# Optimization experiments

Hardware: AMD Instinct MI355X
Metric: run time of the kernel (lower is better)

## Reference

```python
import jax, jax.numpy as jnp
import numpy as np

# config matching init_kwargs
J = 5
Q = 8
T = 15
C = 4
J_PHI = 2
B = 4
N = 65536

# near_sym_b level-1 lowpass (13-tap) from the dtcwt library; highpass via QMF modulation.
H0O = np.array([-0.00455690456024, -0.00543947593727, 0.01702522388155, 0.02382538479492,
                -0.10671180468666, 0.01186609203379, 0.56881042071212, 0.75614564389252,
                0.27529538466888, -0.11720388769911, -0.03887280126882, 0.03466034684485,
                -0.00388321199915], dtype=np.float32)
H1O = (((-1.0) ** np.arange(13)) * H0O[::-1]).astype(np.float32)
# qshift_a 10-tap filters for levels >= 2 (tree b = time-reversed tree a)
H0A = np.array([0.03516384, 0.0, -0.08832942, 0.23389032, 0.76027237,
                0.58751830, 0.0, -0.11430184, 0.0, 0.0], dtype=np.float32)
H0B = H0A[::-1].copy()
H1A = (((-1.0) ** np.arange(10)) * H0B).astype(np.float32)
H1B = H1A[::-1].copy()


def _dwconv(x, h, dilation):
    # depthwise 'same' conv; x: (B,C,N), h: (K,) fixed wavelet filter
    c = x.shape[1]
    k = h.shape[0]
    w = jnp.tile(jnp.asarray(h, x.dtype)[None, None, :], (c, 1, 1))
    tot = dilation * (k - 1)
    return jax.lax.conv_general_dilated(
        x, w, (1,), [(tot // 2, tot - tot // 2)], rhs_dilation=(dilation,),
        dimension_numbers=("NCH", "OIH", "NCH"), feature_group_count=c)


def _gconv(x, w, dilation):
    # grouped learnable conv: x (B,C,N), w (Q*C,1,T), groups=C, 'same' padding
    c = x.shape[1]
    t = w.shape[-1]
    tot = dilation * (t - 1)
    return jax.lax.conv_general_dilated(
        x, w, (1,), [(tot // 2, tot - tot // 2)], rhs_dilation=(dilation,),
        dimension_numbers=("NCH", "OIH", "NCH"), feature_group_count=c)


def _udtcwt(x):
    # undecimated dual-tree CWT (a-trous): returns lowpass and J (real, imag) bandpass pairs
    la, lb = x, x
    bps = []
    for j in range(J):
        d = 1 if j == 0 else 2 ** (j - 1)
        if j == 0:
            h0a, h1a, h0b, h1b = H0O, H1O, H0O, H1O
        else:
            h0a, h1a, h0b, h1b = H0A, H1A, H0B, H1B
        bps.append((_dwconv(la, h1a, d), _dwconv(lb, h1b, d)))
        la = _dwconv(la, h0a, d)
        lb = _dwconv(lb, h0b, d)
    return 0.5 * (la + lb), bps


def _downsample(x):
    # J_phi x (near_sym_b lowpass then ::2 decimation)
    for _ in range(J_PHI):
        x = _dwconv(x, H0O, 1)[:, :, ::2]
    return x


def _forward(x, conv_w, roots, beta):
    lp, bps = _udtcwt(x)
    outs = []
    for j in range(J):
        d = 1 if j == 0 else 2 ** (j - 1)
        scale = 2.0 ** (0.5 * j)  # sqrt(2)**j
        r = _gconv(bps[j][0], conv_w[j], d) / scale
        im = _gconv(bps[j][1], conv_w[j], d) / scale
        u = jnp.sqrt(r * r + im * im)  # ModulusStable
        alpha = jax.nn.sigmoid(roots[j])[None, :, None]  # (1, Q*C, 1)
        u = (jnp.maximum(u, -beta) + beta) ** alpha  # PowerStable
        outs.append(_downsample(u))
    return jnp.concatenate(outs, axis=1)  # (B, C*J*Q, N/2**J_phi)


def setup_inputs() -> dict:
    key = jax.random.key(0)
    kx, kw = jax.random.split(key)
    x = jax.random.normal(kx, (B, C, N), dtype=jnp.float32)
    bound = float(1.0 / np.sqrt(T))  # torch Conv1d default init (in/groups=1)
    conv_w = jax.random.uniform(kw, (J, Q * C, 1, T), dtype=jnp.float32, minval=-bound, maxval=bound)
    roots = jnp.ones((J, Q * C), dtype=jnp.float32)  # module inits root to ones
    beta = jnp.full((1,), 0.01, dtype=jnp.float32)
    return {"x": x, "conv_w": conv_w, "roots": roots, "beta": beta}


def reference(x, conv_w, roots, beta):
    return _forward(x, conv_w, roots, beta)
```

## Files before the change

kernel.cpp:

```cpp
#include <hip/hip_runtime.h>
#include <hip/hip_bf16.h>

typedef float v2f __attribute__((ext_vector_type(2)));

#define B_    4
#define C_    4
#define Q_    8
#define J_    5
#define T_    15
#define NSIG  65536
#define N2SIG 32768
#define NOUT  16384
#define NCH   (B_ * C_)

constexpr float H0Oc[13] = {
    -0.00455690456024f, -0.00543947593727f,  0.01702522388155f,  0.02382538479492f,
    -0.10671180468666f,  0.01186609203379f,  0.56881042071212f,  0.75614564389252f,
     0.27529538466888f, -0.11720388769911f, -0.03887280126882f,  0.03466034684485f,
    -0.00388321199915f };
constexpr float H1Oc[13] = {
    -0.00388321199915f, -0.03466034684485f, -0.03887280126882f,  0.11720388769911f,
     0.27529538466888f, -0.75614564389252f,  0.56881042071212f, -0.01186609203379f,
    -0.10671180468666f, -0.02382538479492f,  0.01702522388155f,  0.00543947593727f,
    -0.00455690456024f };
constexpr float H0Ac[10] = {
     0.03516384f, 0.0f, -0.08832942f, 0.23389032f, 0.76027237f,
     0.58751830f, 0.0f, -0.11430184f, 0.0f, 0.0f };
constexpr float H0Bc[10] = {
     0.0f, 0.0f, -0.11430184f, 0.0f, 0.58751830f,
     0.76027237f, 0.23389032f, -0.08832942f, 0.0f, 0.03516384f };
constexpr float H1Ac[10] = {
     0.0f, 0.0f, -0.11430184f, 0.0f, 0.58751830f,
    -0.76027237f, 0.23389032f, 0.08832942f, 0.0f, -0.03516384f };
constexpr float H1Bc[10] = {
    -0.03516384f, 0.0f, 0.08832942f, 0.23389032f, -0.76027237f,
     0.58751830f, 0.0f, -0.11430184f, 0.0f, 0.0f };

struct Gtab { float v[37]; };
constexpr Gtab make_g() {
    Gtab g{};
    for (int n = 0; n < 37; ++n) {
        float s = 0.f;
        for (int k = 0; k < 13; ++k) {
            int l = n - 2 * k;
            if (l >= 0 && l < 13) s += H0Oc[k] * H0Oc[l];
        }
        g.v[n] = s;
    }
    return g;
}
constexpr Gtab cG = make_g();

#define M2    256
#define NUcnt 1057
#define NUP   1064
#define NBcnt 1169
#define NBP   1176
#define S_    1320

#define SMEM_FLOATS (5280 + 2 * NBP)

__device__ __forceinline__ v2f zmask(v2f a, bool ok) {
    if (!ok) { a.x = 0.f; a.y = 0.f; }
    return a;
}

template<int D>
__device__ __forceinline__ void post_stage(
        const v2f* __restrict__ sRI, v2f* __restrict__ U0, v2f* __restrict__ U1,
        const float* __restrict__ cw, const float* __restrict__ roots,
        float beta, int j, int b, int c, int m0, int mt, int tid,
        float* __restrict__ out) {
    const float lg_is = -0.5f * (float)j;
    const float beta2 = beta * exp2f(0.5f * (float)j);
    const int   u_lo  = 4 * m0 - 18;

    for (int g2 = 0; g2 < 2; ++g2) {
        float w[4][T_], al[4], cq[4];
        #pragma unroll
        for (int qq = 0; qq < 4; ++qq) {
            const int o = c * Q_ + g2 * 4 + qq;
            #pragma unroll
            for (int t = 0; t < T_; t++) w[qq][t] = cw[(size_t)(j * 32 + o) * T_ + t];
            al[qq] = 1.f / (1.f + __expf(-roots[j * 32 + o]));
            cq[qq] = al[qq] * lg_is;
        }

        for (int i = tid; i < NUcnt; i += 256) {
            const int n = u_lo + i;
            const bool ok = ((unsigned)n < (unsigned)NSIG);
            const v2f* tp = sRI + (i + 56 - 7 * D);
            v2f taps[T_];
            #pragma unroll
            for (int t = 0; t < T_; t++) taps[t] = tp[t * D];
            float uq[4];
            #pragma unroll
            for (int qq = 0; qq < 4; ++qq) {
                v2f ri; ri.x = 0.f; ri.y = 0.f;
                #pragma unroll
                for (int t = 0; t < T_; t++) ri += w[qq][t] * taps[t];
                float z2 = fmaf(ri.x, ri.x, ri.y * ri.y);
                float us = sqrtf(z2);
                float lg = __log2f(us + beta2);
                float u  = exp2f(fmaf(al[qq], lg, cq[qq]));
                uq[qq] = ok ? u : 0.f;
            }
            v2f p0; p0.x = uq[0]; p0.y = uq[1];
            v2f p1; p1.x = uq[2]; p1.y = uq[3];
            U0[i] = p0; U1[i] = p1;
        }
        __syncthreads();

        {
            const int m = m0 + tid;
            const bool edge = (mt == 0 && tid < 3) || (mt == 63 && tid >= 253);
            #pragma unroll
            for (int qp = 0; qp < 2; ++qp) {
                const v2f* up = qp ? U1 : U0;
                v2f acc; acc.x = 0.f; acc.y = 0.f;
                #pragma unroll
                for (int n = 0; n < 37; ++n) acc += cG.v[n] * up[4 * tid + n];
                if (edge) {
                    v2f a2; a2.x = 0.f; a2.y = 0.f;
                    for (int k = 0; k < 13; ++k) {
                        int p = 2 * m + k - 6;
                        if (p < 0 || p >= N2SIG) continue;
                        v2f v; v.x = 0.f; v.y = 0.f;
                        for (int l = 0; l < 13; ++l)
                            v += H0Oc[l] * up[4 * tid + 2 * k + l];
                        a2 += H0Oc[k] * v;
                    }
                    acc = a2;
                }
                const int o = c * Q_ + g2 * 4 + 2 * qp;
                out[((size_t)b * 160 + j * 32 + o)     * NOUT + m] = acc.x;
                out[((size_t)b * 160 + j * 32 + o + 1) * NOUT + m] = acc.y;
            }
        }
        __syncthreads();
    }
}

__global__ __launch_bounds__(256, 4) void murenn_all(
        const float* __restrict__ x,
        const float* __restrict__ cw,
        const float* __restrict__ roots,
        const float* __restrict__ beta_p,
        float* __restrict__ out) {
    __shared__ __align__(16) float smem[SMEM_FLOATS];
    float* X   = smem;
    float* L1  = smem + S_;
    v2f*   PP0 = (v2f*)smem;
    v2f*   PP1 = (v2f*)(smem + 2 * S_);
    v2f*   U0  = (v2f*)smem;
    v2f*   U1  = (v2f*)(smem + 2 * NUP);
    v2f*   sRI = (v2f*)(smem + 4 * S_);

    const int tid = threadIdx.x;
    const int mt  = blockIdx.x;
    const int ch  = blockIdx.y;
    const int j   = blockIdx.z;
    const int b   = ch >> 2, c = ch & 3;
    const int m0  = mt * M2;
    const int ofs = 4 * m0 - 147;
    const float beta = beta_p[0];
    const float* xc = x + (size_t)ch * NSIG;

    for (int p = tid; p < S_; p += 256) {
        int g = ofs + p;
        X[p] = ((unsigned)g < (unsigned)NSIG) ? xc[g] : 0.f;
    }
    __syncthreads();

    if (j == 0) {
        for (int i = tid; i < NBcnt; i += 256) {
            int p = 73 + i, g = ofs + p;
            float a = 0.f;
            #pragma unroll
            for (int k = 0; k < 13; k++) a += H1Oc[k] * X[p + k - 6];
            if ((unsigned)g >= (unsigned)NSIG) a = 0.f;
            v2f r; r.x = a; r.y = a;
            sRI[i] = r;
        }
    } else {
        for (int p = 6 + tid; p < 1313; p += 256) {
            int g = ofs + p;
            float a = 0.f;
            #pragma unroll
            for (int k = 0; k < 13; k++) a += H0Oc[k] * X[p + k - 6];
            L1[p] = ((unsigned)g < (unsigned)NSIG) ? a : 0.f;
        }
        __syncthreads();
        if (j == 1) {
            for (int i = tid; i < NBcnt; i += 256) {
                int p = 73 + i, g = ofs + p;
                v2f r; r.x = 0.f; r.y = 0.f;
                #pragma unroll
                for (int k = 0; k < 10; k++) {
                    v2f hk; hk.x = H1Ac[k]; hk.y = H1Bc[k];
                    r += hk * L1[p + k - 4];
                }
                sRI[i] = zmask(r, (unsigned)g < (unsigned)NSIG);
            }
        } else {
            for (int p = 10 + tid; p < 1308; p += 256) {
                int g = ofs + p;
                v2f a; a.x = 0.f; a.y = 0.f;
                #pragma unroll
                for (int k = 0; k < 10; k++) {
                    v2f hk; hk.x = H0Ac[k]; hk.y = H0Bc[k];
                    a += hk * L1[p + k - 4];
                }
                PP1[p] = zmask(a, (unsigned)g < (unsigned)NSIG);
            }
            __syncthreads();
            if (j == 2) {
                for (int i = tid; i < NBcnt; i += 256) {
                    int p = 73 + i, g = ofs + p;
                    v2f r; r.x = 0.f; r.y = 0.f;
                    #pragma unroll
                    for (int k = 0; k < 10; k++) {
                        v2f hk; hk.x = H1Ac[k]; hk.y = H1Bc[k];
                        r += hk * PP1[p + 2 * k - 9];
                    }
                    sRI[i] = zmask(r, (unsigned)g < (unsigned)NSIG);
                }
            } else {
                for (int p = 19 + tid; p < 1299; p += 256) {
                    int g = ofs + p;
                    v2f a; a.x = 0.f; a.y = 0.f;
                    #pragma unroll
                    for (int k = 0; k < 10; k++) {
                        v2f hk; hk.x = H0Ac[k]; hk.y = H0Bc[k];
                        a += hk * PP1[p + 2 * k - 9];
                    }
                    PP0[p] = zmask(a, (unsigned)g < (unsigned)NSIG);
                }
                __syncthreads();
                if (j == 3) {
                    for (int i = tid; i < NBcnt; i += 256) {
                        int p = 73 + i, g = ofs + p;
                        v2f r; r.x = 0.f; r.y = 0.f;
                        #pragma unroll
                        for (int k = 0; k < 10; k++) {
                            v2f hk; hk.x = H1Ac[k]; hk.y = H1Bc[k];
                            r += hk * PP0[p + 4 * k - 18];
                        }
                        sRI[i] = zmask(r, (unsigned)g < (unsigned)NSIG);
                    }
                } else {
                    for (int p = 37 + tid; p < 1281; p += 256) {
                        int g = ofs + p;
                        v2f a; a.x = 0.f; a.y = 0.f;
                        #pragma unroll
                        for (int k = 0; k < 10; k++) {
                            v2f hk; hk.x = H0Ac[k]; hk.y = H0Bc[k];
                            a += hk * PP0[p + 4 * k - 18];
                        }
                        PP1[p] = zmask(a, (unsigned)g < (unsigned)NSIG);
                    }
                    __syncthreads();
                    for (int i = tid; i < NBcnt; i += 256) {
                        int p = 73 + i, g = ofs + p;
                        v2f r; r.x = 0.f; r.y = 0.f;
                        #pragma unroll
                        for (int k = 0; k < 10; k++) {
                            v2f hk; hk.x = H1Ac[k]; hk.y = H1Bc[k];
                            r += hk * PP1[p + 8 * k - 36];
                        }
                        sRI[i] = zmask(r, (unsigned)g < (unsigned)NSIG);
                    }
                }
            }
        }
    }
    __syncthreads();

    if (j == 0)      post_stage<1>(sRI, U0, U1, cw, roots, beta, 0, b, c, m0, mt, tid, out);
    else if (j == 1) post_stage<1>(sRI, U0, U1, cw, roots, beta, 1, b, c, m0, mt, tid, out);
    else if (j == 2) post_stage<2>(sRI, U0, U1, cw, roots, beta, 2, b, c, m0, mt, tid, out);
    else if (j == 3) post_stage<4>(sRI, U0, U1, cw, roots, beta, 3, b, c, m0, mt, tid, out);
    else             post_stage<8>(sRI, U0, U1, cw, roots, beta, 4, b, c, m0, mt, tid, out);
}

extern "C" void kernel_launch(void* const* d_in, const int* in_sizes, int n_in,
                              void* d_out, int out_size, void* d_ws, size_t ws_size,
                              hipStream_t stream) {
    (void)in_sizes; (void)n_in; (void)out_size; (void)d_ws; (void)ws_size;
    const float* x     = (const float*)d_in[0];
    const float* cw    = (const float*)d_in[1];
    const float* roots = (const float*)d_in[2];
    const float* beta  = (const float*)d_in[3];
    float* out = (float*)d_out;

    dim3 grid(NOUT / M2, NCH, J_);
    murenn_all<<<grid, 256, 0, stream>>>(x, cw, roots, beta, out);
}
```

Measured before the change: 184.7 us.

## Process all eight Q filters in one pass with bf16-packed intermediate buffer

The post stage used to run two passes of four filters each, re-reading the taps and syncing twice. It now computes all eight filter outputs per sample in a single pass and stores the modulus-power results as packed bf16 pairs in shared memory, so the buffer still fits. Weights are read straight from global/constant memory instead of being held in registers, and launch bounds drop to 3 blocks per SM. This removes one tap reload and a barrier pass, at the cost of bf16 rounding of the intermediate before the decimation filter and more register pressure.

```diff
diff --git a/kernel.cpp b/kernel.cpp
--- a/kernel.cpp
+++ b/kernel.cpp
@@ -55,7 +55,7 @@
 #define NUcnt 1057
 #define NUP   1064
 #define NBcnt 1169
-#define NBP   1176
+#define NBP   1200
 #define S_    1320
 
 #define SMEM_FLOATS (5280 + 2 * NBP)
@@ -64,84 +64,102 @@
     if (!ok) { a.x = 0.f; a.y = 0.f; }
     return a;
 }
+__device__ __forceinline__ unsigned pack2bf(float a, float b) {
+    unsigned ua = __float_as_uint(a) + 0x8000u;
+    unsigned ub = __float_as_uint(b) + 0x8000u;
+    return (ua >> 16) | (ub & 0xffff0000u);
+}
+__device__ __forceinline__ float unpk_lo(unsigned x) { return __uint_as_float(x << 16); }
+__device__ __forceinline__ float unpk_hi(unsigned x) { return __uint_as_float(x & 0xffff0000u); }
 
 template<int D>
 __device__ __forceinline__ void post_stage(
-        const v2f* __restrict__ sRI, v2f* __restrict__ U0, v2f* __restrict__ U1,
+        const v2f* __restrict__ sRI, uint2* __restrict__ UA, uint2* __restrict__ UB,
         const float* __restrict__ cw, const float* __restrict__ roots,
         float beta, int j, int b, int c, int m0, int mt, int tid,
         float* __restrict__ out) {
     const float lg_is = -0.5f * (float)j;
     const float beta2 = beta * exp2f(0.5f * (float)j);
     const int   u_lo  = 4 * m0 - 18;
-
-    for (int g2 = 0; g2 < 2; ++g2) {
-        float w[4][T_], al[4], cq[4];
+    const float* wbase = cw + (size_t)(j * 32 + c * 8) * T_;
+
+    float al[8], cq[8];
+    #pragma unroll
+    for (int q = 0; q < 8; ++q) {
+        al[q] = 1.f / (1.f + __expf(-roots[j * 32 + c * 8 + q]));
+        cq[q] = al[q] * lg_is;
+    }
+
+    for (int i = tid; i < NUcnt; i += 256) {
+        const int n = u_lo + i;
+        const bool ok = ((unsigned)n < (unsigned)NSIG);
+        const v2f* tp = sRI + (i + 56 - 7 * D);
+        v2f tap[T_];
         #pragma unroll
-        for (int qq = 0; qq < 4; ++qq) {
-            const int o = c * Q_ + g2 * 4 + qq;
+        for (int t = 0; t < T_; t++) tap[t] = tp[t * D];
+        float uq[8];
+        #pragma unroll
+        for (int q = 0; q < 8; ++q) {
+            v2f ri; ri.x = 0.f; ri.y = 0.f;
             #pragma unroll
-            for (int t = 0; t < T_; t++) w[qq][t] = cw[(size_t)(j * 32 + o) * T_ + t];
-            al[qq] = 1.f / (1.f + __expf(-roots[j * 32 + o]));
-            cq[qq] = al[qq] * lg_is;
-        }
-
-        for (int i = tid; i < NUcnt; i += 256) {
-            const int n = u_lo + i;
-            const bool ok = ((unsigned)n < (unsigned)NSIG);
-            const v2f* tp = sRI + (i + 56 - 7 * D);
-            v2f taps[T_];
+            for (int t = 0; t < T_; t++) ri += wbase[q * T_ + t] * tap[t];
+            float z2 = fmaf(ri.x, ri.x, ri.y * ri.y);
+            float us = sqrtf(z2);
+            float lg = __log2f(us + beta2);
+            float u  = exp2f(fmaf(al[q], lg, cq[q]));
+            uq[q] = ok ? u : 0.f;
+        }
+        uint2 pa, pb;
+        pa.x = pack2bf(uq[0], uq[1]); pa.y = pack2bf(uq[2], uq[3]);
+        pb.x = pack2bf(uq[4], uq[5]); pb.y = pack2bf(uq[6], uq[7]);
+        UA[i] = pa; UB[i] = pb;
+    }
+    __syncthreads();
+
+    {
+        const int m = m0 + tid;
+        const bool edge = (mt == 0 && tid < 3) || (mt == 63 && tid >= 253);
+        #pragma unroll
+        for (int pl = 0; pl < 2; ++pl) {
+            const uint2* up = pl ? UB : UA;
+            float a0 = 0.f, a1 = 0.f, a2 = 0.f, a3 = 0.f;
             #pragma unroll
-            for (int t = 0; t < T_; t++) taps[t] = tp[t * D];
-            float uq[4];
-            #pragma unroll
-            for (int qq = 0; qq < 4; ++qq) {
-                v2f ri; ri.x = 0.f; ri.y = 0.f;
-                #pragma unroll
-                for (int t = 0; t < T_; t++) ri += w[qq][t] * taps[t];
-                float z2 = fmaf(ri.x, ri.x, ri.y * ri.y);
-                float us = sqrtf(z2);
-                float lg = __log2f(us + beta2);
-                float u  = exp2f(fmaf(al[qq], lg, cq[qq]));
-                uq[qq] = ok ? u : 0.f;
-            }
-            v2f p0; p0.x = uq[0]; p0.y = uq[1];
-            v2f p1; p1.x = uq[2]; p1.y = uq[3];
-            U0[i] = p0; U1[i] = p1;
-        }
-        __syncthreads();
-
-        {
-            const int m = m0 + tid;
-            const bool edge = (mt == 0 && tid < 3) || (mt == 63 && tid >= 253);
-            #pragma unroll
-            for (int qp = 0; qp < 2; ++qp) {
-                const v2f* up = qp ? U1 : U0;
-                v2f acc; acc.x = 0.f; acc.y = 0.f;
-                #pragma unroll
-                for (int n = 0; n < 37; ++n) acc += cG.v[n] * up[4 * tid + n];
-                if (edge) {
-                    v2f a2; a2.x = 0.f; a2.y = 0.f;
-                    for (int k = 0; k < 13; ++k) {
-                        int p = 2 * m + k - 6;
-                        if (p < 0 || p >= N2SIG) continue;
-                        v2f v; v.x = 0.f; v.y = 0.f;
-                        for (int l = 0; l < 13; ++l)
-                            v += H0Oc[l] * up[4 * tid + 2 * k + l];
-                        a2 += H0Oc[k] * v;
-                    }
-                    acc = a2;
-                }
-                const int o = c * Q_ + g2 * 4 + 2 * qp;
-                out[((size_t)b * 160 + j * 32 + o)     * NOUT + m] = acc.x;
-                out[((size_t)b * 160 + j * 32 + o + 1) * NOUT + m] = acc.y;
-            }
-        }
-        __syncthreads();
-    }
-}
-
-__global__ __launch_bounds__(256, 4) void murenn_all(
+            for (int nn = 0; nn < 37; ++nn) {
+                uint2 t = up[4 * tid + nn];
+                a0 = fmaf(cG.v[nn], unpk_lo(t.x), a0);
+                a1 = fmaf(cG.v[nn], unpk_hi(t.x), a1);
+                a2 = fmaf(cG.v[nn], unpk_lo(t.y), a2);
+                a3 = fmaf(cG.v[nn], unpk_hi(t.y), a3);
+            }
+            if (edge) {
+                float e0 = 0.f, e1 = 0.f, e2 = 0.f, e3 = 0.f;
+                for (int k = 0; k < 13; ++k) {
+                    int p = 2 * m + k - 6;
+                    if (p < 0 || p >= N2SIG) continue;
+                    float v0 = 0.f, v1 = 0.f, v2 = 0.f, v3 = 0.f;
+                    for (int l = 0; l < 13; ++l) {
+                        uint2 t = up[4 * tid + 2 * k + l];
+                        v0 = fmaf(H0Oc[l], unpk_lo(t.x), v0);
+                        v1 = fmaf(H0Oc[l], unpk_hi(t.x), v1);
+                        v2 = fmaf(H0Oc[l], unpk_lo(t.y), v2);
+                        v3 = fmaf(H0Oc[l], unpk_hi(t.y), v3);
+                    }
+                    e0 = fmaf(H0Oc[k], v0, e0); e1 = fmaf(H0Oc[k], v1, e1);
+                    e2 = fmaf(H0Oc[k], v2, e2); e3 = fmaf(H0Oc[k], v3, e3);
+                }
+                a0 = e0; a1 = e1; a2 = e2; a3 = e3;
+            }
+            const int o = c * Q_ + pl * 4;
+            float* ob = out + ((size_t)b * 160 + j * 32 + o) * NOUT + m;
+            ob[0]        = a0;
+            ob[NOUT]     = a1;
+            ob[2 * NOUT] = a2;
+            ob[3 * NOUT] = a3;
+        }
+    }
+}
+
+__global__ __launch_bounds__(256, 3) void murenn_all(
         const float* __restrict__ x,
         const float* __restrict__ cw,
         const float* __restrict__ roots,
@@ -152,8 +170,8 @@
     float* L1  = smem + S_;
     v2f*   PP0 = (v2f*)smem;
     v2f*   PP1 = (v2f*)(smem + 2 * S_);
-    v2f*   U0  = (v2f*)smem;
-    v2f*   U1  = (v2f*)(smem + 2 * NUP);
+    uint2* UA  = (uint2*)smem;
+    uint2* UB  = (uint2*)(smem + 2 * NUP);
     v2f*   sRI = (v2f*)(smem + 4 * S_);
 
     const int tid = threadIdx.x;
@@ -276,11 +294,11 @@
     }
     __syncthreads();
 
-    if (j == 0)      post_stage<1>(sRI, U0, U1, cw, roots, beta, 0, b, c, m0, mt, tid, out);
-    else if (j == 1) post_stage<1>(sRI, U0, U1, cw, roots, beta, 1, b, c, m0, mt, tid, out);
-    else if (j == 2) post_stage<2>(sRI, U0, U1, cw, roots, beta, 2, b, c, m0, mt, tid, out);
-    else if (j == 3) post_stage<4>(sRI, U0, U1, cw, roots, beta, 3, b, c, m0, mt, tid, out);
-    else             post_stage<8>(sRI, U0, U1, cw, roots, beta, 4, b, c, m0, mt, tid, out);
+    if (j == 0)      post_stage<1>(sRI, UA, UB, cw, roots, beta, 0, b, c, m0, mt, tid, out);
+    else if (j == 1) post_stage<1>(sRI, UA, UB, cw, roots, beta, 1, b, c, m0, mt, tid, out);
+    else if (j == 2) post_stage<2>(sRI, UA, UB, cw, roots, beta, 2, b, c, m0, mt, tid, out);
+    else if (j == 3) post_stage<4>(sRI, UA, UB, cw, roots, beta, 3, b, c, m0, mt, tid, out);
+    else             post_stage<8>(sRI, UA, UB, cw, roots, beta, 4, b, c, m0, mt, tid, out);
 }
 
 extern "C" void kernel_launch(void* const* d_in, const int* in_sizes, int n_in,
```

Result: slower. 211.1 us (+14.3%).
